# Optimization experiments

Measured on AMD Instinct MI355X. Metric: run time of the kernel, lower is better.

Reference implementation:

```python
import jax, jax.numpy as jnp
import numpy as np

N, IN_FEATURES, OUT_FEATURES = 131072, 128, 512


def setup_inputs() -> dict:
    key = jax.random.key(0)
    k1, k2 = jax.random.split(key)
    x = jax.random.normal(k1, (N, IN_FEATURES), dtype=jnp.float32)
    centers = jax.random.normal(k2, (OUT_FEATURES, IN_FEATURES), dtype=jnp.float32)  # nn.init.normal_(0,1)
    log_sigmas = jnp.zeros((OUT_FEATURES,), dtype=jnp.float32)  # nn.init.constant_(0)
    return {"x": x, "centers": centers, "log_sigmas": log_sigmas}


def reference(x, centers, log_sigmas):
    # (N, out, in) expanded intermediate of the torch code; same math).
    x_sq = jnp.sum(x * x, axis=-1, keepdims=True)            # (N, 1)
    c_sq = jnp.sum(centers * centers, axis=-1)               # (out,)
    cross = x @ centers.T                                    # (N, out) GEMM
    d2 = jnp.maximum(x_sq - 2.0 * cross + c_sq[None, :], 0.0)
    distances = jnp.sqrt(d2) / jnp.exp(log_sigmas)[None, :]  # (N, out)
    # gaussian basis: phi(r) = exp(-r^2)
    return jnp.exp(-(distances * distances))
```

## Files before the change

kernel.cpp:

```cpp
#include <hip/hip_runtime.h>
#include <hip/hip_bf16.h>


typedef __attribute__((ext_vector_type(8))) short bf16x8;
typedef __attribute__((ext_vector_type(4))) float f32x4;
typedef __attribute__((ext_vector_type(4))) unsigned u32x4;

#define KDIM 128
#define ODIM 512
#define LOG2E 1.4426950408889634f

union BF8 { unsigned u[4]; bf16x8 v; u32x4 q; };

__device__ __forceinline__ unsigned pack_bf2(float a, float b) {
    unsigned ua = __builtin_bit_cast(unsigned, a);
    unsigned ub = __builtin_bit_cast(unsigned, b);
    ua += 0x7fffu + ((ua >> 16) & 1u);
    ub += 0x7fffu + ((ub >> 16) & 1u);
    return (ua >> 16) | (ub & 0xffff0000u);
}

__global__ __launch_bounds__(256) void rbf_pack_kernel(
    const float* __restrict__ centers,
    const float* __restrict__ log_sigmas,
    u32x4* __restrict__ wsfrag,
    float* __restrict__ wsis,
    float* __restrict__ wscs)
{
    const int b = blockIdx.x;
    if (b < 32) {
        int i  = b * 256 + threadIdx.x;
        int g  = i >> 8;
        int kk = (i >> 6) & 3;
        int l  = i & 63;
        int c  = g * 16 + (l & 15);
        int k0 = kk * 32 + (l >> 4) * 8;
        const f32x4* p = (const f32x4*)(centers + (size_t)c * KDIM + k0);
        f32x4 v0 = p[0], v1 = p[1];
        BF8 w;
        w.u[0] = pack_bf2(v0.x, v0.y);
        w.u[1] = pack_bf2(v0.z, v0.w);
        w.u[2] = pack_bf2(v1.x, v1.y);
        w.u[3] = pack_bf2(v1.z, v1.w);
        wsfrag[i] = w.q;
    } else {
        int c = (b - 32) * 256 + threadIdx.x;
        const f32x4* p = (const f32x4*)(centers + (size_t)c * KDIM);
        float s = 0.f;
        #pragma unroll
        for (int k = 0; k < 32; ++k) {
            f32x4 v = p[k];
            s += v.x*v.x + v.y*v.y + v.z*v.z + v.w*v.w;
        }
        float a = __expf(-2.0f * log_sigmas[c]) * LOG2E;
        wsis[c] = a;
        wscs[c] = s * a;
    }
}

__global__ __launch_bounds__(256, 4) void rbf_main_kernel(
    const float* __restrict__ x,
    const u32x4* __restrict__ wsfrag,
    const f32x4* __restrict__ wsis4,
    const f32x4* __restrict__ wscs4,
    float* __restrict__ out)
{
    __shared__ f32x4 stage[4][32 * 16];

    const int t  = threadIdx.x;
    const int w  = t >> 6;
    const int l  = t & 63;
    const int lr = l & 15;
    const int lk = l >> 4;

    const int r0 = blockIdx.x * 128 + w * 32;

    bf16x8 xf0[4], xf1[4];
    float xsq0, xsq1;
#define LOADX(XF, XS, ROWOFF)                                                  \
    {                                                                          \
        const float* xp = x + (size_t)(r0 + (ROWOFF) + lr) * KDIM + lk * 8;    \
        float s = 0.f;                                                         \
        _Pragma("unroll")                                                      \
        for (int kk = 0; kk < 4; ++kk) {                                       \
            const f32x4* p = (const f32x4*)(xp + kk * 32);                     \
            f32x4 v0 = p[0], v1 = p[1];                                        \
            s += v0.x*v0.x + v0.y*v0.y + v0.z*v0.z + v0.w*v0.w                 \
               + v1.x*v1.x + v1.y*v1.y + v1.z*v1.z + v1.w*v1.w;                \
            BF8 bw;                                                            \
            bw.u[0] = pack_bf2(v0.x, v0.y);                                    \
            bw.u[1] = pack_bf2(v0.z, v0.w);                                    \
            bw.u[2] = pack_bf2(v1.x, v1.y);                                    \
            bw.u[3] = pack_bf2(v1.z, v1.w);                                    \
            XF[kk] = bw.v;                                                     \
        }                                                                      \
        s += __shfl_xor(s, 16);                                                \
        s += __shfl_xor(s, 32);                                                \
        XS = s;                                                                \
    }
    LOADX(xf0, xsq0, 0)
    LOADX(xf1, xsq1, 16)
#undef LOADX

    f32x4* st = &stage[w][0];
    const bf16x8* fb = (const bf16x8*)wsfrag + l;

    bf16x8 cfA[4], cfB[4];
    cfA[0] = fb[0];
    cfA[1] = fb[64];
    cfA[2] = fb[128];
    cfA[3] = fb[192];

#define STEP(G, T, CUR, NXT)                                                   \
    {                                                                          \
        const int gn = ((G) + 1) & 31;                                         \
        NXT[0] = fb[gn * 256 + 0];                                             \
        NXT[1] = fb[gn * 256 + 64];                                            \
        NXT[2] = fb[gn * 256 + 128];                                           \
        NXT[3] = fb[gn * 256 + 192];                                           \
        f32x4 a0 = (f32x4){0.f, 0.f, 0.f, 0.f};                                \
        f32x4 a1 = (f32x4){0.f, 0.f, 0.f, 0.f};                                \
        _Pragma("unroll")                                                      \
        for (int kk = 0; kk < 4; ++kk) {                                       \
            a0 = __builtin_amdgcn_mfma_f32_16x16x32_bf16(CUR[kk], xf0[kk], a0, 0, 0, 0); \
            a1 = __builtin_amdgcn_mfma_f32_16x16x32_bf16(CUR[kk], xf1[kk], a1, 0, 0, 0); \
        }                                                                      \
        const int gi = (G) * 4 + lk;                                           \
        f32x4 A4 = wsis4[gi];                                                  \
        f32x4 B4 = wscs4[gi];                                                  \
        f32x4 o0, o1;                                                          \
        o0.x = exp2f(-fmaxf(fmaf(A4.x, fmaf(-2.f, a0[0], xsq0), B4.x), 0.f));  \
        o0.y = exp2f(-fmaxf(fmaf(A4.y, fmaf(-2.f, a0[1], xsq0), B4.y), 0.f));  \
        o0.z = exp2f(-fmaxf(fmaf(A4.z, fmaf(-2.f, a0[2], xsq0), B4.z), 0.f));  \
        o0.w = exp2f(-fmaxf(fmaf(A4.w, fmaf(-2.f, a0[3], xsq0), B4.w), 0.f));  \
        o1.x = exp2f(-fmaxf(fmaf(A4.x, fmaf(-2.f, a1[0], xsq1), B4.x), 0.f));  \
        o1.y = exp2f(-fmaxf(fmaf(A4.y, fmaf(-2.f, a1[1], xsq1), B4.y), 0.f));  \
        o1.z = exp2f(-fmaxf(fmaf(A4.z, fmaf(-2.f, a1[2], xsq1), B4.z), 0.f));  \
        o1.w = exp2f(-fmaxf(fmaf(A4.w, fmaf(-2.f, a1[3], xsq1), B4.w), 0.f));  \
        const int ch = ((T) * 4 + lk) ^ lr;         \
        st[lr * 16 + ch]        = o0;                         \
        st[(16 + lr) * 16 + ch] = o1;              \
    }

    #pragma unroll 1
    for (int G0 = 0; G0 < 32; G0 += 4) {
        STEP(G0 + 0, 0, cfA, cfB)
        STEP(G0 + 1, 1, cfB, cfA)
        STEP(G0 + 2, 2, cfA, cfB)
        STEP(G0 + 3, 3, cfB, cfA)

        #pragma unroll
        for (int q = 0; q < 8; ++q) {
            int row = (q & 3) * 8 + (l >> 3);
            int c   = (q >> 2) * 8 + (l & 7);
            f32x4 v = st[row * 16 + (c ^ (row & 15))];
            float* op = out + (size_t)(r0 + row) * ODIM + G0 * 16 + c * 4;
            *(f32x4*)op = v;
        }
    }
#undef STEP
}

__global__ __launch_bounds__(1024, 1) void rbf_fallback_kernel(
    const float* __restrict__ x,
    const float* __restrict__ centers,
    const float* __restrict__ log_sigmas,
    float* __restrict__ out)
{
    __shared__ u32x4 sC[ODIM * 16];
    __shared__ float sIS[ODIM];
    __shared__ float sCS[ODIM];

    const int t  = threadIdx.x;
    const int w  = t >> 6;
    const int l  = t & 63;
    const int lr = l & 15;
    const int lk = l >> 4;

    #pragma unroll
    for (int i = 0; i < 8; ++i) {
        int c    = i * 1024 + t;
        int row  = c >> 4;
        int col8 = c & 15;
        const f32x4* gp = (const f32x4*)(centers + (size_t)row * KDIM + col8 * 8);
        f32x4 v0 = gp[0], v1 = gp[1];
        float s = v0.x*v0.x + v0.y*v0.y + v0.z*v0.z + v0.w*v0.w
                + v1.x*v1.x + v1.y*v1.y + v1.z*v1.z + v1.w*v1.w;
        s += __shfl_xor(s, 1); s += __shfl_xor(s, 2);
        s += __shfl_xor(s, 4); s += __shfl_xor(s, 8);
        BF8 wv;
        wv.u[0] = pack_bf2(v0.x, v0.y);
        wv.u[1] = pack_bf2(v0.z, v0.w);
        wv.u[2] = pack_bf2(v1.x, v1.y);
        wv.u[3] = pack_bf2(v1.z, v1.w);
        int byte = row * 256 + col8 * 16;
        byte ^= (row & 7) << 4;
        *(u32x4*)((char*)sC + byte) = wv.q;
        if ((t & 15) == 0) {
            float a = __expf(-2.0f * log_sigmas[row]);
            sIS[row] = a;
            sCS[row] = s * a;
        }
    }
    __syncthreads();

    const int r0 = blockIdx.x * 512 + w * 32;
    bf16x8 xf[2][4];
    float  xsq[2];
    #pragma unroll
    for (int tt = 0; tt < 2; ++tt) {
        const float* xp = x + (size_t)(r0 + tt * 16 + lr) * KDIM + lk * 8;
        float s = 0.f;
        #pragma unroll
        for (int kk = 0; kk < 4; ++kk) {
            const f32x4* p = (const f32x4*)(xp + kk * 32);
            f32x4 v0 = p[0], v1 = p[1];
            s += v0.x*v0.x + v0.y*v0.y + v0.z*v0.z + v0.w*v0.w
               + v1.x*v1.x + v1.y*v1.y + v1.z*v1.z + v1.w*v1.w;
            BF8 b;
            b.u[0] = pack_bf2(v0.x, v0.y);
            b.u[1] = pack_bf2(v0.z, v0.w);
            b.u[2] = pack_bf2(v1.x, v1.y);
            b.u[3] = pack_bf2(v1.z, v1.w);
            xf[tt][kk] = b.v;
        }
        s += __shfl_xor(s, 16);
        s += __shfl_xor(s, 32);
        xsq[tt] = s;
    }

    float* orow0 = out + (size_t)(r0 + lr) * ODIM;
    float* orow1 = out + (size_t)(r0 + 16 + lr) * ODIM;

    #pragma unroll 2
    for (int g = 0; g < 32; ++g) {
        bf16x8 af[4];
        #pragma unroll
        for (int kk = 0; kk < 4; ++kk) {
            int row  = g * 16 + lr;
            int byte = row * 256 + kk * 64 + lk * 16;
            byte ^= (row & 7) << 4;
            af[kk] = *(const bf16x8*)((const char*)sC + byte);
        }
        f32x4 a0 = (f32x4){0.f, 0.f, 0.f, 0.f};
        f32x4 a1 = (f32x4){0.f, 0.f, 0.f, 0.f};
        #pragma unroll
        for (int kk = 0; kk < 4; ++kk) {
            a0 = __builtin_amdgcn_mfma_f32_16x16x32_bf16(af[kk], xf[0][kk], a0, 0, 0, 0);
            a1 = __builtin_amdgcn_mfma_f32_16x16x32_bf16(af[kk], xf[1][kk], a1, 0, 0, 0);
        }
        const int cb = g * 16 + lk * 4;
        f32x4 A4 = *(const f32x4*)&sIS[cb];
        f32x4 B4 = *(const f32x4*)&sCS[cb];
        f32x4 o0, o1;
        o0.x = __expf(-fmaxf(fmaf(A4.x, fmaf(-2.f, a0[0], xsq[0]), B4.x), 0.f));
        o0.y = __expf(-fmaxf(fmaf(A4.y, fmaf(-2.f, a0[1], xsq[0]), B4.y), 0.f));
        o0.z = __expf(-fmaxf(fmaf(A4.z, fmaf(-2.f, a0[2], xsq[0]), B4.z), 0.f));
        o0.w = __expf(-fmaxf(fmaf(A4.w, fmaf(-2.f, a0[3], xsq[0]), B4.w), 0.f));
        o1.x = __expf(-fmaxf(fmaf(A4.x, fmaf(-2.f, a1[0], xsq[1]), B4.x), 0.f));
        o1.y = __expf(-fmaxf(fmaf(A4.y, fmaf(-2.f, a1[1], xsq[1]), B4.y), 0.f));
        o1.z = __expf(-fmaxf(fmaf(A4.z, fmaf(-2.f, a1[2], xsq[1]), B4.z), 0.f));
        o1.w = __expf(-fmaxf(fmaf(A4.w, fmaf(-2.f, a1[3], xsq[1]), B4.w), 0.f));
        *(f32x4*)(orow0 + cb) = o0;
        *(f32x4*)(orow1 + cb) = o1;
    }
}

extern "C" void kernel_launch(void* const* d_in, const int* in_sizes, int n_in,
                              void* d_out, int out_size, void* d_ws, size_t ws_size,
                              hipStream_t stream) {
    const float* x          = (const float*)d_in[0];
    const float* centers    = (const float*)d_in[1];
    const float* log_sigmas = (const float*)d_in[2];
    float* out = (float*)d_out;

    const int n_rows = in_sizes[0] / KDIM;

    const size_t WS_NEED = 128 * 1024 + 2 * 2048;
    if (ws_size >= WS_NEED) {
        u32x4* wsfrag = (u32x4*)d_ws;
        float* wsis   = (float*)((char*)d_ws + 128 * 1024);
        float* wscs   = (float*)((char*)d_ws + 128 * 1024 + 2048);
        rbf_pack_kernel<<<34, 256, 0, stream>>>(centers, log_sigmas,
                                                wsfrag, wsis, wscs);
        rbf_main_kernel<<<n_rows / 128, 256, 0, stream>>>(
            x, wsfrag, (const f32x4*)wsis, (const f32x4*)wscs, out);
    } else {
        rbf_fallback_kernel<<<n_rows / 512, 1024, 0, stream>>>(
            x, centers, log_sigmas, out);
    }
}
```

Before: 86.46 us.

## Split output columns across waves and write full contiguous 32-row tiles

Each block now covers 32 rows instead of 128. The four waves split the 512 output columns, each wave taking 8 groups of 16 centers, where before each wave looped over all columns for its own rows. All results are staged into a 64 KB shared tile, and after one barrier the block writes the contiguous 32x512 output region with fully coalesced stores. This gives longer store bursts and four times as many blocks. The cost is that every wave redundantly loads and converts the same 32 x rows, LDS use per block grows, which lowers occupancy (launch bounds drop to 2), and the store phase no longer overlaps compute within the block.

```diff
diff --git a/kernel.cpp b/kernel.cpp
--- a/kernel.cpp
+++ b/kernel.cpp
@@ -58,14 +58,14 @@
     }
 }
 
-__global__ __launch_bounds__(256, 4) void rbf_main_kernel(
+__global__ __launch_bounds__(256, 2) void rbf_main_kernel(
     const float* __restrict__ x,
     const u32x4* __restrict__ wsfrag,
     const f32x4* __restrict__ wsis4,
     const f32x4* __restrict__ wscs4,
-    float* __restrict__ out)
+    f32x4* __restrict__ out4)
 {
-    __shared__ f32x4 stage[4][32 * 16];
+    __shared__ f32x4 stage[32 * 128];
 
     const int t  = threadIdx.x;
     const int w  = t >> 6;
@@ -73,7 +73,7 @@
     const int lr = l & 15;
     const int lk = l >> 4;
 
-    const int r0 = blockIdx.x * 128 + w * 32;
+    const int r0 = blockIdx.x * 32;
 
     bf16x8 xf0[4], xf1[4];
     float xsq0, xsq1;
@@ -102,18 +102,21 @@
     LOADX(xf1, xsq1, 16)
 #undef LOADX
 
-    f32x4* st = &stage[w][0];
     const bf16x8* fb = (const bf16x8*)wsfrag + l;
 
     bf16x8 cfA[4], cfB[4];
-    cfA[0] = fb[0];
-    cfA[1] = fb[64];
-    cfA[2] = fb[128];
-    cfA[3] = fb[192];
-
-#define STEP(G, T, CUR, NXT)                                                   \
+    {
+        const int g0 = w * 8;
+        cfA[0] = fb[g0 * 256 + 0];
+        cfA[1] = fb[g0 * 256 + 64];
+        cfA[2] = fb[g0 * 256 + 128];
+        cfA[3] = fb[g0 * 256 + 192];
+    }
+
+#define STEP(GG, CUR, NXT)                                                     \
     {                                                                          \
-        const int gn = ((G) + 1) & 31;                                         \
+        const int G  = w * 8 + (GG);                                           \
+        const int gn = w * 8 + (((GG) + 1) & 7);                               \
         NXT[0] = fb[gn * 256 + 0];                                             \
         NXT[1] = fb[gn * 256 + 64];                                            \
         NXT[2] = fb[gn * 256 + 128];                                           \
@@ -125,7 +128,7 @@
             a0 = __builtin_amdgcn_mfma_f32_16x16x32_bf16(CUR[kk], xf0[kk], a0, 0, 0, 0); \
             a1 = __builtin_amdgcn_mfma_f32_16x16x32_bf16(CUR[kk], xf1[kk], a1, 0, 0, 0); \
         }                                                                      \
-        const int gi = (G) * 4 + lk;                                           \
+        const int gi = G * 4 + lk;                                             \
         f32x4 A4 = wsis4[gi];                                                  \
         f32x4 B4 = wscs4[gi];                                                  \
         f32x4 o0, o1;                                                          \
@@ -137,28 +140,31 @@
         o1.y = exp2f(-fmaxf(fmaf(A4.y, fmaf(-2.f, a1[1], xsq1), B4.y), 0.f));  \
         o1.z = exp2f(-fmaxf(fmaf(A4.z, fmaf(-2.f, a1[2], xsq1), B4.z), 0.f));  \
         o1.w = exp2f(-fmaxf(fmaf(A4.w, fmaf(-2.f, a1[3], xsq1), B4.w), 0.f));  \
-        const int ch = ((T) * 4 + lk) ^ lr;         \
-        st[lr * 16 + ch]        = o0;                         \
-        st[(16 + lr) * 16 + ch] = o1;              \
-    }
-
-    #pragma unroll 1
-    for (int G0 = 0; G0 < 32; G0 += 4) {
-        STEP(G0 + 0, 0, cfA, cfB)
-        STEP(G0 + 1, 1, cfB, cfA)
-        STEP(G0 + 2, 2, cfA, cfB)
-        STEP(G0 + 3, 3, cfB, cfA)
-
-        #pragma unroll
-        for (int q = 0; q < 8; ++q) {
-            int row = (q & 3) * 8 + (l >> 3);
-            int c   = (q >> 2) * 8 + (l & 7);
-            f32x4 v = st[row * 16 + (c ^ (row & 15))];
-            float* op = out + (size_t)(r0 + row) * ODIM + G0 * 16 + c * 4;
-            *(f32x4*)op = v;
-        }
-    }
+        const int c = (G * 4 + lk) ^ (lr & 7);              \
+        stage[lr * 128 + c]        = o0;                      \
+        stage[(16 + lr) * 128 + c] = o1;                      \
+    }
+
+    STEP(0, cfA, cfB)
+    STEP(1, cfB, cfA)
+    STEP(2, cfA, cfB)
+    STEP(3, cfB, cfA)
+    STEP(4, cfA, cfB)
+    STEP(5, cfB, cfA)
+    STEP(6, cfA, cfB)
+    STEP(7, cfB, cfA)
 #undef STEP
+
+    __syncthreads();
+
+    f32x4* op = out4 + (size_t)blockIdx.x * 4096;
+    #pragma unroll
+    for (int i = 0; i < 16; ++i) {
+        int j   = i * 256 + t;
+        int row = j >> 7;
+        int cl  = j & 127;
+        op[j] = stage[row * 128 + (cl ^ (row & 7))];
+    }
 }
 
 __global__ __launch_bounds__(1024, 1) void rbf_fallback_kernel(
@@ -272,7 +278,6 @@
     const float* x          = (const float*)d_in[0];
     const float* centers    = (const float*)d_in[1];
     const float* log_sigmas = (const float*)d_in[2];
-    float* out = (float*)d_out;
 
     const int n_rows = in_sizes[0] / KDIM;
 
@@ -283,10 +288,10 @@
         float* wscs   = (float*)((char*)d_ws + 128 * 1024 + 2048);
         rbf_pack_kernel<<<34, 256, 0, stream>>>(centers, log_sigmas,
                                                 wsfrag, wsis, wscs);
-        rbf_main_kernel<<<n_rows / 128, 256, 0, stream>>>(
-            x, wsfrag, (const f32x4*)wsis, (const f32x4*)wscs, out);
+        rbf_main_kernel<<<n_rows / 32, 256, 0, stream>>>(
+            x, wsfrag, (const f32x4*)wsis, (const f32x4*)wscs, (f32x4*)d_out);
     } else {
         rbf_fallback_kernel<<<n_rows / 512, 1024, 0, stream>>>(
-            x, centers, log_sigmas, out);
-    }
-}
+            x, centers, log_sigmas, (float*)d_out);
+    }
+}
```

Result: slower. 104.4 us (+20.7%).
